# Kernel tuning notes

Hardware: AMD Instinct MI355X
Metric: run time of the kernel (lower is better)

The kernel has to match this reference:

```python
import jax, jax.numpy as jnp
import numpy as np

H, W = 1024, 1024
K = 15            # degree_max / neighbour_nb
GAMMA = 0.5
MULTIPLIER = 1.0
WIN = 4           # half window for neighbor offsets (window_size=9)


def setup_inputs() -> dict:
    key = jax.random.key(0)
    k1, k2, k3, k4, k5 = jax.random.split(key, 5)
    N = H * W
    sig1 = jax.random.normal(k1, (1, 1, H, W), dtype=jnp.float32)
    sig2 = jax.random.normal(k2, (1, 2, H, W), dtype=jnp.float32)
    weights = jax.random.uniform(k3, (K, N), dtype=jnp.float32)
    # Build a local-window neighbor graph, as similarity_graph would produce.
    idx = jnp.arange(N, dtype=jnp.int32)
    y = idx // W
    x = idx % W
    dy = jax.random.randint(k4, (K, N), -WIN, WIN + 1, dtype=jnp.int32)
    dx = jax.random.randint(k5, (K, N), -WIN, WIN + 1, dtype=jnp.int32)
    yn = jnp.clip(y[None] + dy, 0, H - 1)
    xn = jnp.clip(x[None] + dx, 0, W - 1)
    neighbours = (yn * W + xn).astype(jnp.int32)            # (K, N)
    # dist = (x_source - x_target, y_source - y_target), per constructor.
    dist = jnp.stack([(x[None] - xn), (y[None] - yn)], axis=1).astype(jnp.float32)  # (K, 2, N)
    return {"sig1": sig1, "sig2": sig2, "weights": weights, "dist": dist,
            "neighbours": neighbours}


def reference(sig1, sig2, weights, dist, neighbours):
    N = weights.shape[1]
    s1 = sig1.reshape(-1)                 # (N,)
    s2 = sig2.reshape(2, -1)              # (2, N)
    # planar term: sum_c sig2[c, n] * dist[k, c, n]  -> (K, N)
    plane = jnp.einsum('cn,kcn->kn', s2, dist)
    aux1 = s1[None, :] - s1[neighbours] - plane           # (K, N)
    aux1 = jnp.sqrt(jnp.sum((aux1 * weights) ** 2, axis=0)).sum()
    # vector-field difference: (K, 2, N), norm over channel dim
    diff2 = s2[None, :, :] - jnp.transpose(s2[:, neighbours], (1, 0, 2))
    aux2 = jnp.sqrt(jnp.sum(diff2 * diff2, axis=1))        # (K, N)
    aux2 = jnp.sum(aux2 * weights)
    loss = (aux1 + GAMMA * aux2) / N
    return MULTIPLIER * loss
```

## Files before the change

### kernel.cpp

```cpp
#include <hip/hip_runtime.h>
#include <hip/hip_bf16.h>

#define HH 1024
#define WW 1024
#define NN (HH * WW)
#define KK 15
#define GAMMA_F 0.5f

#define TR 12
#define TW 136

__device__ __forceinline__ void cp16(const float* g, float* l) {
    __builtin_amdgcn_global_load_lds(
        (const __attribute__((address_space(1))) void*)g,
        (__attribute__((address_space(3))) void*)l, 16, 0, 0);
}

__global__ __launch_bounds__(256) void ppr_kernel(
    const float* __restrict__ s1,
    const float* __restrict__ s2,
    const float* __restrict__ w,
    const int* __restrict__ nb,
    float* __restrict__ out)
{
    __shared__ __align__(16) float t1 [TR * TW];
    __shared__ __align__(16) float t2a[TR * TW];
    __shared__ __align__(16) float t2b[TR * TW];
    __shared__ float smem[4];

    const int tid  = threadIdx.x;
    const int wv   = tid >> 6;
    const int lane = tid & 63;
    const int ty   = blockIdx.x >> 3;
    const int tx   = blockIdx.x & 7;
    const int y0   = ty << 2;
    const int c0   = tx << 7;
    const int yc   = y0 + wv;
    const int xc0  = c0 + (lane << 1);
    const int n    = yc * WW + xc0;

    int2   j2[KK];
    float2 w2[KK];
#pragma unroll
    for (int k = 0; k < KK; ++k) j2[k] = *(const int2*)(nb + (size_t)k * NN + n);
#pragma unroll
    for (int k = 0; k < KK; ++k) w2[k] = *(const float2*)(w + (size_t)k * NN + n);

    int xs = c0 - 4, dof = 0, nl = 34;
    if (tx == 0)      { xs = 0; dof = 4; nl = 33; }
    else if (tx == 7) { nl = 33; }

#pragma unroll
    for (int it = 0; it < 9; ++it) {
        const int t   = wv * 9 + it;
        const int arr = t / 12;
        const int rr  = t - arr * 12;
        int gy = y0 - 4 + rr;
        gy = gy < 0 ? 0 : (gy > HH - 1 ? HH - 1 : gy);
        const float* src =
            (arr == 0 ? s1 : (arr == 1 ? s2 : s2 + NN)) + (size_t)gy * WW + xs;
        float* dst = (arr == 0 ? t1 : (arr == 1 ? t2a : t2b)) + rr * TW + dof;
        if (lane < nl) cp16(src + lane * 4, dst);
    }

    __builtin_amdgcn_sched_barrier(0);
    __syncthreads();

    const int own0 = (wv + 4) * TW + (lane << 1) + 4;
    const float s1n_0 = t1 [own0],     s1n_1 = t1 [own0 + 1];
    const float s2a_0 = t2a[own0],     s2a_1 = t2a[own0 + 1];
    const float s2b_0 = t2b[own0],     s2b_1 = t2b[own0 + 1];

    const int cbase = (4 - y0) * TW + 4 - c0;

    float acc1_0 = 0.f, acc2_0 = 0.f, acc1_1 = 0.f, acc2_1 = 0.f;
#pragma unroll
    for (int k = 0; k < KK; ++k) {
        {
            const int jj = j2[k].x;
            const int yn = jj >> 10;
            const int xn = jj & (WW - 1);
            const int off = yn * TW + xn + cbase;
            const float g1  = t1 [off];
            const float g2a = t2a[off];
            const float g2b = t2b[off];
            const float d0 = (float)(xc0 - xn);
            const float d1 = (float)(yc  - yn);
            const float wkk = w2[k].x;
            const float plane = fmaf(s2a_0, d0, s2b_0 * d1);
            const float a1 = (s1n_0 - g1 - plane) * wkk;
            acc1_0 = fmaf(a1, a1, acc1_0);
            const float e0 = s2a_0 - g2a;
            const float e1 = s2b_0 - g2b;
            acc2_0 = fmaf(sqrtf(fmaf(e0, e0, e1 * e1)), wkk, acc2_0);
        }
        {
            const int jj = j2[k].y;
            const int yn = jj >> 10;
            const int xn = jj & (WW - 1);
            const int off = yn * TW + xn + cbase;
            const float g1  = t1 [off];
            const float g2a = t2a[off];
            const float g2b = t2b[off];
            const float d0 = (float)(xc0 + 1 - xn);
            const float d1 = (float)(yc - yn);
            const float wkk = w2[k].y;
            const float plane = fmaf(s2a_1, d0, s2b_1 * d1);
            const float a1 = (s1n_1 - g1 - plane) * wkk;
            acc1_1 = fmaf(a1, a1, acc1_1);
            const float e0 = s2a_1 - g2a;
            const float e1 = s2b_1 - g2b;
            acc2_1 = fmaf(sqrtf(fmaf(e0, e0, e1 * e1)), wkk, acc2_1);
        }
    }
    float local = sqrtf(acc1_0) + sqrtf(acc1_1)
                + GAMMA_F * (acc2_0 + acc2_1);

#pragma unroll
    for (int off2 = 32; off2 > 0; off2 >>= 1)
        local += __shfl_down(local, off2, 64);

    if (lane == 0) smem[wv] = local;
    __syncthreads();

    if (tid == 0) {
        const float s = smem[0] + smem[1] + smem[2] + smem[3];
        atomicAdd(out, s * (1.0f / (float)NN));
    }
}

extern "C" void kernel_launch(void* const* d_in, const int* in_sizes, int n_in,
                              void* d_out, int out_size, void* d_ws, size_t ws_size,
                              hipStream_t stream) {
    const float* s1   = (const float*)d_in[0];
    const float* s2   = (const float*)d_in[1];
    const float* w    = (const float*)d_in[2];
    const int*   nb   = (const int*)d_in[4];
    float* out = (float*)d_out;

    hipMemsetAsync(out, 0, sizeof(float) * (size_t)out_size, stream);

    const int block = 256;
    const int grid  = NN / (block * 2);
    ppr_kernel<<<grid, block, 0, stream>>>(s1, s2, w, nb, out);
}
```

Before: 248.0 us.

## Split neighbour/weight loads around tile sync and replace atomic with two-pass reduce

Neighbour indices and weights for the first 8 k are loaded before the halo-tile copy, and the remaining 7 only after the barrier. This cuts register pressure and overlaps part of the global traffic with the LDS tile fill. The plane term is rewritten so a per-pixel constant is hoisted out of the k loop, and tile copies are reorganised by array and row. The memset plus per-block atomicAdd is replaced by per-block partials in workspace and a second single-block reduction kernel, which adds one extra launch.

```diff
diff --git a/kernel.cpp b/kernel.cpp
--- a/kernel.cpp
+++ b/kernel.cpp
@@ -9,6 +9,7 @@
 
 #define TR 12
 #define TW 136
+#define NBLK (NN / 512)
 
 __device__ __forceinline__ void cp16(const float* g, float* l) {
     __builtin_amdgcn_global_load_lds(
@@ -21,7 +22,7 @@
     const float* __restrict__ s2,
     const float* __restrict__ w,
     const int* __restrict__ nb,
-    float* __restrict__ out)
+    float* __restrict__ partial)
 {
     __shared__ __align__(16) float t1 [TR * TW];
     __shared__ __align__(16) float t2a[TR * TW];
@@ -37,84 +38,99 @@
     const int c0   = tx << 7;
     const int yc   = y0 + wv;
     const int xc0  = c0 + (lane << 1);
-    const int n    = yc * WW + xc0;
+    const int n    = (yc << 10) + xc0;
 
-    int2   j2[KK];
-    float2 w2[KK];
+    int2   jA[8];
+    float2 wA[8];
 #pragma unroll
-    for (int k = 0; k < KK; ++k) j2[k] = *(const int2*)(nb + (size_t)k * NN + n);
+    for (int k = 0; k < 8; ++k) jA[k] = *(const int2*)(nb + (size_t)k * NN + n);
 #pragma unroll
-    for (int k = 0; k < KK; ++k) w2[k] = *(const float2*)(w + (size_t)k * NN + n);
+    for (int k = 0; k < 8; ++k) wA[k] = *(const float2*)(w + (size_t)k * NN + n);
 
     int xs = c0 - 4, dof = 0, nl = 34;
     if (tx == 0)      { xs = 0; dof = 4; nl = 33; }
     else if (tx == 7) { nl = 33; }
+    const bool on = (lane < nl);
 
+    const float* const srcs[3] = { s1, s2, s2 + NN };
+    float* const       dsts[3] = { t1, t2a, t2b };
 #pragma unroll
-    for (int it = 0; it < 9; ++it) {
-        const int t   = wv * 9 + it;
-        const int arr = t / 12;
-        const int rr  = t - arr * 12;
-        int gy = y0 - 4 + rr;
-        gy = gy < 0 ? 0 : (gy > HH - 1 ? HH - 1 : gy);
-        const float* src =
-            (arr == 0 ? s1 : (arr == 1 ? s2 : s2 + NN)) + (size_t)gy * WW + xs;
-        float* dst = (arr == 0 ? t1 : (arr == 1 ? t2a : t2b)) + rr * TW + dof;
-        if (lane < nl) cp16(src + lane * 4, dst);
+    for (int arr = 0; arr < 3; ++arr) {
+#pragma unroll
+        for (int r3 = 0; r3 < 3; ++r3) {
+            const int rr = wv + (r3 << 2);
+            int gy = y0 - 4 + rr;
+            gy = gy < 0 ? 0 : (gy > HH - 1 ? HH - 1 : gy);
+            if (on) cp16(srcs[arr] + (size_t)gy * WW + xs + lane * 4,
+                         dsts[arr] + rr * TW + dof);
+        }
     }
 
     __builtin_amdgcn_sched_barrier(0);
     __syncthreads();
 
+    int2   jB[7];
+    float2 wB[7];
+#pragma unroll
+    for (int k = 0; k < 7; ++k)
+        jB[k] = *(const int2*)(nb + (size_t)(k + 8) * NN + n);
+#pragma unroll
+    for (int k = 0; k < 7; ++k)
+        wB[k] = *(const float2*)(w + (size_t)(k + 8) * NN + n);
+    __builtin_amdgcn_sched_barrier(0);
+
     const int own0 = (wv + 4) * TW + (lane << 1) + 4;
-    const float s1n_0 = t1 [own0],     s1n_1 = t1 [own0 + 1];
-    const float s2a_0 = t2a[own0],     s2a_1 = t2a[own0 + 1];
-    const float s2b_0 = t2b[own0],     s2b_1 = t2b[own0 + 1];
+    const float s1n_0 = t1 [own0], s1n_1 = t1 [own0 + 1];
+    const float sa_0  = t2a[own0], sa_1  = t2a[own0 + 1];
+    const float sb_0  = t2b[own0], sb_1  = t2b[own0 + 1];
+
+    const float ycf = (float)yc;
+    const float D0 = s1n_0 - fmaf(sa_0, (float)xc0,       sb_0 * ycf);
+    const float D1 = s1n_1 - fmaf(sa_1, (float)(xc0 + 1), sb_1 * ycf);
 
     const int cbase = (4 - y0) * TW + 4 - c0;
 
     float acc1_0 = 0.f, acc2_0 = 0.f, acc1_1 = 0.f, acc2_1 = 0.f;
-#pragma unroll
-    for (int k = 0; k < KK; ++k) {
+
+    auto body = [&](int2 j2, float2 w2) {
         {
-            const int jj = j2[k].x;
+            const unsigned jj = (unsigned)j2.x;
             const int yn = jj >> 10;
             const int xn = jj & (WW - 1);
             const int off = yn * TW + xn + cbase;
             const float g1  = t1 [off];
             const float g2a = t2a[off];
             const float g2b = t2b[off];
-            const float d0 = (float)(xc0 - xn);
-            const float d1 = (float)(yc  - yn);
-            const float wkk = w2[k].x;
-            const float plane = fmaf(s2a_0, d0, s2b_0 * d1);
-            const float a1 = (s1n_0 - g1 - plane) * wkk;
+            const float P  = fmaf(sa_0, (float)xn, sb_0 * (float)yn);
+            const float a1 = (D0 + (P - g1)) * w2.x;
             acc1_0 = fmaf(a1, a1, acc1_0);
-            const float e0 = s2a_0 - g2a;
-            const float e1 = s2b_0 - g2b;
-            acc2_0 = fmaf(sqrtf(fmaf(e0, e0, e1 * e1)), wkk, acc2_0);
+            const float e0 = sa_0 - g2a;
+            const float e1 = sb_0 - g2b;
+            acc2_0 = fmaf(sqrtf(fmaf(e0, e0, e1 * e1)), w2.x, acc2_0);
         }
         {
-            const int jj = j2[k].y;
+            const unsigned jj = (unsigned)j2.y;
             const int yn = jj >> 10;
             const int xn = jj & (WW - 1);
             const int off = yn * TW + xn + cbase;
             const float g1  = t1 [off];
             const float g2a = t2a[off];
             const float g2b = t2b[off];
-            const float d0 = (float)(xc0 + 1 - xn);
-            const float d1 = (float)(yc - yn);
-            const float wkk = w2[k].y;
-            const float plane = fmaf(s2a_1, d0, s2b_1 * d1);
-            const float a1 = (s1n_1 - g1 - plane) * wkk;
+            const float P  = fmaf(sa_1, (float)xn, sb_1 * (float)yn);
+            const float a1 = (D1 + (P - g1)) * w2.y;
             acc1_1 = fmaf(a1, a1, acc1_1);
-            const float e0 = s2a_1 - g2a;
-            const float e1 = s2b_1 - g2b;
-            acc2_1 = fmaf(sqrtf(fmaf(e0, e0, e1 * e1)), wkk, acc2_1);
+            const float e0 = sa_1 - g2a;
+            const float e1 = sb_1 - g2b;
+            acc2_1 = fmaf(sqrtf(fmaf(e0, e0, e1 * e1)), w2.y, acc2_1);
         }
-    }
-    float local = sqrtf(acc1_0) + sqrtf(acc1_1)
-                + GAMMA_F * (acc2_0 + acc2_1);
+    };
+
+#pragma unroll
+    for (int k = 0; k < 8; ++k) body(jA[k], wA[k]);
+#pragma unroll
+    for (int k = 0; k < 7; ++k) body(jB[k], wB[k]);
+
+    float local = sqrtf(acc1_0) + sqrtf(acc1_1) + GAMMA_F * (acc2_0 + acc2_1);
 
 #pragma unroll
     for (int off2 = 32; off2 > 0; off2 >>= 1)
@@ -123,10 +139,27 @@
     if (lane == 0) smem[wv] = local;
     __syncthreads();
 
-    if (tid == 0) {
-        const float s = smem[0] + smem[1] + smem[2] + smem[3];
-        atomicAdd(out, s * (1.0f / (float)NN));
-    }
+    if (tid == 0)
+        partial[blockIdx.x] = smem[0] + smem[1] + smem[2] + smem[3];
+}
+
+__global__ __launch_bounds__(256) void ppr_reduce(
+    const float* __restrict__ partial, float* __restrict__ out)
+{
+    const int tid = threadIdx.x;
+    const float4 a = ((const float4*)partial)[tid];
+    const float4 b = ((const float4*)partial)[tid + 256];
+    float v = (a.x + a.y) + (a.z + a.w) + (b.x + b.y) + (b.z + b.w);
+
+#pragma unroll
+    for (int off = 32; off > 0; off >>= 1)
+        v += __shfl_down(v, off, 64);
+
+    __shared__ float sm[4];
+    if ((tid & 63) == 0) sm[tid >> 6] = v;
+    __syncthreads();
+    if (tid == 0)
+        out[0] = (sm[0] + sm[1] + sm[2] + sm[3]) * (1.0f / (float)NN);
 }
 
 extern "C" void kernel_launch(void* const* d_in, const int* in_sizes, int n_in,
@@ -136,11 +169,9 @@
     const float* s2   = (const float*)d_in[1];
     const float* w    = (const float*)d_in[2];
     const int*   nb   = (const int*)d_in[4];
-    float* out = (float*)d_out;
+    float* out     = (float*)d_out;
+    float* partial = (float*)d_ws;
 
-    hipMemsetAsync(out, 0, sizeof(float) * (size_t)out_size, stream);
-
-    const int block = 256;
-    const int grid  = NN / (block * 2);
-    ppr_kernel<<<grid, block, 0, stream>>>(s1, s2, w, nb, out);
+    ppr_kernel<<<NBLK, 256, 0, stream>>>(s1, s2, w, nb, partial);
+    ppr_reduce<<<1, 256, 0, stream>>>(partial, out);
 }
```

Measured after the change: 244.2 us. About the same (-1.5%).
